# Optimization experiments

Hardware: AMD Instinct MI355X
Metric: run time of the kernel (lower is better)

Reference implementation:

```python
import jax, jax.numpy as jnp
import numpy as np

MAX_REL = 128  # max_relative_position


def setup_inputs() -> dict:
    key = jax.random.key(0)
    k1, k2, k3, k4 = jax.random.split(key, 4)
    B, H, S, D = 2, 8, 2048, 64
    q = jax.random.normal(k1, (B, H, S, D), dtype=jnp.float32)
    k = jax.random.normal(k2, (B, H, S, D), dtype=jnp.float32)
    v = jax.random.normal(k3, (B, H, S, D), dtype=jnp.float32)
    rel_table = jax.random.normal(k4, (2 * MAX_REL + 1, D), dtype=jnp.float32)
    return {"q": q, "k": k, "v": v, "rel_table": rel_table}


def reference(q, k, v, rel_table):
    B, H, S, D = q.shape
    scale = jnp.sqrt(jnp.asarray(D, q.dtype))
    # content scores: [B,H,S,S]
    qk_scores = jnp.einsum('bhqd,bhkd->bhqk', q, k)
    # relative position index matrix [S,S] clamped to [-MAX_REL, MAX_REL]
    pos = jnp.arange(S)
    rel_idx = jnp.clip(pos[None, :] - pos[:, None], -MAX_REL, MAX_REL) + MAX_REL
    rel_emb = rel_table[rel_idx]  # [S,S,D]
    # relative scores: per-query dot with rel embedding row -> [B,H,S,S]
    rel_scores = jnp.einsum('bhqd,qkd->bhqk', q, rel_emb)
    scores = (qk_scores + rel_scores) / scale
    attn = jax.nn.softmax(scores, axis=-1)
    # output: [B,H,S,D]
    return jnp.einsum('bhqk,bhkd->bhqd', attn, v)
```

## Files before the change

kernel.cpp:

```cpp
#include <hip/hip_runtime.h>

typedef _Float16 half8 __attribute__((ext_vector_type(8)));
typedef _Float16 half4 __attribute__((ext_vector_type(4)));
typedef float f32x4 __attribute__((ext_vector_type(4)));

#define S_LEN 2048
#define HDIM 64
#define QBLK 64
#define KVBLK 64
#define NT (S_LEN / KVBLK)
#define QRS 258
#define NBH 16
#define L2E 1.44269504f
#define TSTR 72

__device__ __forceinline__ void load_lds16(const void* g, void* l) {
    __builtin_amdgcn_global_load_lds(
        (const __attribute__((address_space(1))) unsigned int*)g,
        (__attribute__((address_space(3))) unsigned int*)l, 16, 0, 0);
}

__global__ __launch_bounds__(256)
void convert_kv_kernel(const float* __restrict__ Kg, const float* __restrict__ Vg,
                       _Float16* __restrict__ Kh, _Float16* __restrict__ Vp)
{
    __shared__ _Float16 tile[KVBLK * TSTR];
    const int bid = blockIdx.x;
    const int tid = threadIdx.x;
    if (bid < 1024) {
        const int id = bid * 256 + tid;
        const int r  = id >> 3;
        const int d0 = (id & 7) * 8;
        const float* src = Kg + (size_t)r * HDIM + d0;
        f32x4 f0 = *(const f32x4*)(src);
        f32x4 f1 = *(const f32x4*)(src + 4);
        half8 h;
#pragma unroll
        for (int j = 0; j < 4; ++j) { h[j] = (_Float16)f0[j]; h[j+4] = (_Float16)f1[j]; }
        const int bh = r >> 11, kvg = r & 2047;
        const int t = kvg >> 6, kv = kvg & 63;
        const size_t blk = (size_t)(bh * NT + t) * 8192;
        const int off = (kv * 128 + d0 * 2) ^ ((kv & 7) << 4);
        *(half8*)((char*)Kh + blk + off) = h;
    } else {
        const int bt = bid - 1024;
        const int bh = bt >> 5, t = bt & 31;
        {
            const int kv = tid >> 2;
            const int d0 = (tid & 3) * 16;
            const float* src = Vg + ((size_t)bh * S_LEN + t * KVBLK + kv) * HDIM + d0;
            f32x4 f0 = *(const f32x4*)(src);
            f32x4 f1 = *(const f32x4*)(src + 4);
            f32x4 f2 = *(const f32x4*)(src + 8);
            f32x4 f3 = *(const f32x4*)(src + 12);
            half8 h0, h1;
#pragma unroll
            for (int j = 0; j < 4; ++j) {
                h0[j] = (_Float16)f0[j]; h0[j+4] = (_Float16)f1[j];
                h1[j] = (_Float16)f2[j]; h1[j+4] = (_Float16)f3[j];
            }
            *(half8*)&tile[kv * TSTR + d0]     = h0;
            *(half8*)&tile[kv * TSTR + d0 + 8] = h1;
        }
        __syncthreads();
        {
            const int dp = tid >> 2;
            const int u0 = (tid & 3) * 2;
            char* base = (char*)Vp + (size_t)bt * 8192;
            const int dsw = (dp & 7) << 4;
#pragma unroll
            for (int ui = 0; ui < 2; ++ui) {
                const int u  = u0 + ui;
                const int kc = u >> 2, gg = u & 3;
                half8 ch;
#pragma unroll
                for (int r = 0; r < 4; ++r) {
                    ch[r]     = tile[(32*kc + 4*gg + r)      * TSTR + dp];
                    ch[4 + r] = tile[(32*kc + 16 + 4*gg + r) * TSTR + dp];
                }
                *(half8*)(base + ((dp * 128 + u * 16) ^ dsw)) = ch;
            }
        }
    }
}

__global__ __launch_bounds__(512, 4)
void relattn_v8(const float* __restrict__ Qg, const float* __restrict__ RELg,
                const _Float16* __restrict__ Kh, const _Float16* __restrict__ Vp,
                float* __restrict__ Og)
{
    __shared__ __attribute__((aligned(16))) _Float16 Kbuf[3][4096];
    __shared__ __attribute__((aligned(16))) _Float16 Vbuf[2][4096];
    __shared__ __attribute__((aligned(16))) _Float16 Qrel[QBLK * QRS];
    __shared__ float MLds[2][64];
    __shared__ float LLds[2][64];

    const int tid  = threadIdx.x;
    const int wave = tid >> 6;
    const int lane = tid & 63;
    const int c  = lane & 15;
    const int g  = lane >> 4;
    const int qs = wave & 3;
    const int ks = wave >> 2;

    const int wk = ((blockIdx.x & 7) << 6) + (blockIdx.x >> 3);
    const int bh = wk >> 5;
    const int q0 = (wk & 31) * QBLK;
    const size_t hoff = (size_t)bh * S_LEN * HDIM;

    const char* kimg = (const char*)Kh + (size_t)bh * NT * 8192;
    const char* vimg = (const char*)Vp + (size_t)bh * NT * 8192;

    load_lds16(vimg + tid * 16, (char*)Vbuf + tid * 16);
    load_lds16(kimg + tid * 16, (char*)Kbuf + tid * 16);
    load_lds16(kimg + 8192 + tid * 16, (char*)&Kbuf[1][0] + tid * 16);

    const int qb0 = q0 + 16 * qs;
    half8 bq[2];
#pragma unroll
    for (int kc = 0; kc < 2; ++kc) {
        const float* src = Qg + hoff + (size_t)(qb0 + c) * HDIM + kc * 32 + g * 8;
        f32x4 f0 = *(const f32x4*)(src);
        f32x4 f1 = *(const f32x4*)(src + 4);
        half8 h;
#pragma unroll
        for (int j = 0; j < 4; ++j) {
            h[j]     = (_Float16)(f0[j] * 0.125f);
            h[j + 4] = (_Float16)(f1[j] * 0.125f);
        }
        bq[kc] = h;
    }

    if (ks == 0) {
#pragma unroll 1
        for (int t = 0; t < 17; ++t) {
            f32x4 acc = {0.f, 0.f, 0.f, 0.f};
            int r = t * 16 + c;
            if (r > 256) r = 256;
#pragma unroll
            for (int kc = 0; kc < 2; ++kc) {
                const float* src = RELg + (size_t)r * HDIM + kc * 32 + g * 8;
                f32x4 f0 = *(const f32x4*)(src);
                f32x4 f1 = *(const f32x4*)(src + 4);
                half8 b;
#pragma unroll
                for (int j = 0; j < 4; ++j) { b[j] = (_Float16)f0[j]; b[j+4] = (_Float16)f1[j]; }
                acc = __builtin_amdgcn_mfma_f32_16x16x32_f16(bq[kc], b, acc, 0, 0, 0);
            }
            const int col = t * 16 + c;
            if (col <= 256) {
#pragma unroll
                for (int reg = 0; reg < 4; ++reg)
                    Qrel[(16 * qs + 4 * g + reg) * QRS + col] = (_Float16)acc[reg];
            }
        }
    }
    __syncthreads();

    const _Float16* qr = &Qrel[(16 * qs + c) * QRS];
    const float bias_lo = (float)qr[0];
    const float bias_hi = (float)qr[256];

    const int swz = (c & 7) << 4;
    int akoff[2][2], voff[4];
#pragma unroll
    for (int n = 0; n < 2; ++n)
#pragma unroll
        for (int kc = 0; kc < 2; ++kc)
            akoff[n][kc] = (((32 * ks + 16 * n + c) * 128) + kc * 64 + g * 16) ^ swz;
#pragma unroll
    for (int dn = 0; dn < 4; ++dn)
        voff[dn] = (((16 * dn + c) * 128) + ks * 64 + g * 16) ^ swz;

    half8 ones;
#pragma unroll
    for (int j = 0; j < 8; ++j) ones[j] = (_Float16)1.0f;

    float m = -1e30f;
    f32x4 l_acc = {0.f, 0.f, 0.f, 0.f};
    f32x4 oacc[4];
#pragma unroll
    for (int i = 0; i < 4; ++i) oacc[i] = (f32x4){0.f, 0.f, 0.f, 0.f};

#define BODY(t, KB, VB, VBN, KBN) do {                                               \
        asm volatile("s_waitcnt vmcnt(1)" ::: "memory");                             \
        __builtin_amdgcn_s_barrier();                                                \
        {                                                                            \
            const int tv = ((t) + 1 < NT) ? (t) + 1 : NT - 1;                        \
            const int tk = ((t) + 2 < NT) ? (t) + 2 : NT - 1;                        \
            load_lds16(vimg + (size_t)tv * 8192 + tid * 16,                          \
                       (char*)&Vbuf[VBN][0] + tid * 16);                             \
            load_lds16(kimg + (size_t)tk * 8192 + tid * 16,                          \
                       (char*)&Kbuf[KBN][0] + tid * 16);                             \
        }                                                                            \
        const char* kb = (const char*)&Kbuf[KB][0];                                  \
        const char* vb = (const char*)&Vbuf[VB][0];                                  \
        const int kws = (t) * KVBLK + 32 * ks;                                       \
        half8 a00 = *(const half8*)(kb + akoff[0][0]);                               \
        half8 a01 = *(const half8*)(kb + akoff[0][1]);                               \
        half8 a10 = *(const half8*)(kb + akoff[1][0]);                               \
        half8 a11 = *(const half8*)(kb + akoff[1][1]);                               \
        f32x4 s0 = {0.f,0.f,0.f,0.f}, s1 = {0.f,0.f,0.f,0.f};                        \
        __builtin_amdgcn_s_setprio(1);                                               \
        s0 = __builtin_amdgcn_mfma_f32_16x16x32_f16(a00, bq[0], s0, 0, 0, 0);        \
        s1 = __builtin_amdgcn_mfma_f32_16x16x32_f16(a10, bq[0], s1, 0, 0, 0);        \
        s0 = __builtin_amdgcn_mfma_f32_16x16x32_f16(a01, bq[1], s0, 0, 0, 0);        \
        s1 = __builtin_amdgcn_mfma_f32_16x16x32_f16(a11, bq[1], s1, 0, 0, 0);        \
        __builtin_amdgcn_s_setprio(0);                                               \
        float bias = 0.f;                                                            \
        float lm;                                                                    \
        if (kws + 159 <= qb0) {                                                      \
            bias = bias_lo;                                                          \
            lm = fmaxf(fmaxf(fmaxf(s0[0], s0[1]), fmaxf(s0[2], s0[3])),              \
                       fmaxf(fmaxf(s1[0], s1[1]), fmaxf(s1[2], s1[3]))) + bias;      \
        } else if (kws >= qb0 + 143) {                                               \
            bias = bias_hi;                                                          \
            lm = fmaxf(fmaxf(fmaxf(s0[0], s0[1]), fmaxf(s0[2], s0[3])),              \
                       fmaxf(fmaxf(s1[0], s1[1]), fmaxf(s1[2], s1[3]))) + bias;      \
        } else {                                                                     \
            const int base_d = kws + 4 * g - (qb0 + c) + 128;                        \
            _Pragma("unroll")                                                        \
            for (int r = 0; r < 4; ++r) {                                            \
                int i0 = base_d + r;                                                 \
                i0 = i0 < 0 ? 0 : (i0 > 256 ? 256 : i0);                             \
                int i1 = base_d + 16 + r;                                            \
                i1 = i1 < 0 ? 0 : (i1 > 256 ? 256 : i1);                             \
                s0[r] += (float)qr[i0];                                              \
                s1[r] += (float)qr[i1];                                              \
            }                                                                        \
            lm = fmaxf(fmaxf(fmaxf(s0[0], s0[1]), fmaxf(s0[2], s0[3])),              \
                       fmaxf(fmaxf(s1[0], s1[1]), fmaxf(s1[2], s1[3])));             \
        }                                                                            \
        if (!__all(lm <= m + 8.f)) {                                                 \
            float mt = lm;                                                           \
            mt = fmaxf(mt, __shfl_xor(mt, 16, 64));                                  \
            mt = fmaxf(mt, __shfl_xor(mt, 32, 64));                                  \
            const float mnew = fmaxf(m, mt);                                         \
            const float al = __builtin_amdgcn_exp2f((m - mnew) * L2E);               \
            m = mnew;                                                                \
            _Pragma("unroll")                                                        \
            for (int r = 0; r < 4; ++r) {                                            \
                const float ar = __shfl(al, 20 * g + r, 64);                         \
                l_acc[r] *= ar;                                                      \
                _Pragma("unroll")                                                    \
                for (int dn = 0; dn < 4; ++dn) oacc[dn][r] *= ar;                    \
            }                                                                        \
        }                                                                            \
        const float fold = (bias - m) * L2E;                                         \
        half8 ap;                                                                    \
        _Pragma("unroll")                                                            \
        for (int r = 0; r < 4; ++r) {                                                \
            ap[r]     = (_Float16)__builtin_amdgcn_exp2f(fmaf(s0[r], L2E, fold));    \
            ap[4 + r] = (_Float16)__builtin_amdgcn_exp2f(fmaf(s1[r], L2E, fold));    \
        }                                                                            \
        half8 v0 = *(const half8*)(vb + voff[0]);                                    \
        half8 v1 = *(const half8*)(vb + voff[1]);                                    \
        half8 v2 = *(const half8*)(vb + voff[2]);                                    \
        half8 v3 = *(const half8*)(vb + voff[3]);                                    \
        __builtin_amdgcn_s_setprio(1);                                               \
        l_acc   = __builtin_amdgcn_mfma_f32_16x16x32_f16(ap, ones, l_acc, 0, 0, 0);  \
        oacc[0] = __builtin_amdgcn_mfma_f32_16x16x32_f16(ap, v0, oacc[0], 0, 0, 0);  \
        oacc[1] = __builtin_amdgcn_mfma_f32_16x16x32_f16(ap, v1, oacc[1], 0, 0, 0);  \
        oacc[2] = __builtin_amdgcn_mfma_f32_16x16x32_f16(ap, v2, oacc[2], 0, 0, 0);  \
        oacc[3] = __builtin_amdgcn_mfma_f32_16x16x32_f16(ap, v3, oacc[3], 0, 0, 0);  \
        __builtin_amdgcn_s_setprio(0);                                               \
    } while (0)

#pragma unroll 1
    for (int tt = 0; tt < 30; tt += 6) {
        BODY(tt + 0, 0, 0, 1, 2);
        BODY(tt + 1, 1, 1, 0, 0);
        BODY(tt + 2, 2, 0, 1, 1);
        BODY(tt + 3, 0, 1, 0, 2);
        BODY(tt + 4, 1, 0, 1, 0);
        BODY(tt + 5, 2, 1, 0, 1);
    }
    BODY(30, 0, 0, 1, 2);
    BODY(31, 1, 1, 0, 0);
#undef BODY

    asm volatile("s_waitcnt vmcnt(0)" ::: "memory");
    __syncthreads();

    {
        char* Ob = (char*)Kbuf;
#pragma unroll
        for (int r = 0; r < 4; ++r) {
            const int row = 16 * qs + 4 * g + r;
            const int rsw = (row & 7) << 4;
#pragma unroll
            for (int dn = 0; dn < 4; ++dn)
                *(_Float16*)(Ob + ks * 8192 + ((row * 128 + (16 * dn + c) * 2) ^ rsw))
                    = (_Float16)oacc[dn][r];
        }
        if (g == 0) MLds[ks][16 * qs + c] = m;
        if (c == 0) {
#pragma unroll
            for (int r = 0; r < 4; ++r)
                LLds[ks][16 * qs + 4 * g + r] = l_acc[r];
        }
        __syncthreads();

        const int row = 16 * qs + c;
        const int rsw = (c & 7) << 4;
        const float m0 = MLds[0][row], m1 = MLds[1][row];
        const float l0 = LLds[0][row], l1 = LLds[1][row];
        const float M  = fmaxf(m0, m1);
        const float w0 = __builtin_amdgcn_exp2f((m0 - M) * L2E);
        const float w1 = __builtin_amdgcn_exp2f((m1 - M) * L2E);
        const float inv = 1.0f / (l0 * w0 + l1 * w1);

        const int dof = 64 * ks + 16 * g;
        half8 o0 = *(const half8*)(Ob +        ((row * 128 + dof) ^ rsw));
        half8 o1 = *(const half8*)(Ob + 8192 + ((row * 128 + dof) ^ rsw));
        float* dst = Og + hoff + (size_t)(q0 + row) * HDIM + 32 * ks + 8 * g;
        f32x4 oA, oB;
#pragma unroll
        for (int j = 0; j < 4; ++j) {
            oA[j] = ((float)o0[j]     * w0 + (float)o1[j]     * w1) * inv;
            oB[j] = ((float)o0[4 + j] * w0 + (float)o1[4 + j] * w1) * inv;
        }
        *(f32x4*)dst = oA;
        *(f32x4*)(dst + 4) = oB;
    }
}

__global__ __launch_bounds__(256, 2)
void relattn_v1(const float* __restrict__ Qg, const float* __restrict__ Kg,
                const float* __restrict__ Vg, const float* __restrict__ RELg,
                float* __restrict__ Og)
{
    __shared__ _Float16 Klds[KVBLK * HDIM];
    __shared__ _Float16 Vt[HDIM * KVBLK];
    __shared__ _Float16 Plds[4][16 * KVBLK];
    __shared__ _Float16 Qrel[QBLK * QRS];

    const int tid  = threadIdx.x;
    const int wave = tid >> 6;
    const int lane = tid & 63;
    const int c = lane & 15;
    const int g = lane >> 4;

    const int bid = blockIdx.x;
    const int bh  = bid >> 5;
    const int q0  = (bid & 31) * QBLK;

    const size_t hoff = (size_t)bh * S_LEN * HDIM;
    const float* Qh = Qg + hoff;
    const float* Kh = Kg + hoff;
    const float* Vh = Vg + hoff;

    const int qrow_frag = q0 + wave * 16 + c;
    half8 aq[2];
#pragma unroll
    for (int kc = 0; kc < 2; ++kc) {
        const float* src = Qh + (size_t)qrow_frag * HDIM + kc * 32 + g * 8;
        f32x4 f0 = *(const f32x4*)(src);
        f32x4 f1 = *(const f32x4*)(src + 4);
        half8 h;
#pragma unroll
        for (int j = 0; j < 4; ++j) {
            h[j]     = (_Float16)(f0[j] * 0.125f);
            h[j + 4] = (_Float16)(f1[j] * 0.125f);
        }
        aq[kc] = h;
    }

#pragma unroll 1
    for (int t = 0; t < 17; ++t) {
        f32x4 acc = {0.f, 0.f, 0.f, 0.f};
        int r = t * 16 + c;
        if (r > 256) r = 256;
#pragma unroll
        for (int kc = 0; kc < 2; ++kc) {
            const float* src = RELg + (size_t)r * HDIM + kc * 32 + g * 8;
            f32x4 f0 = *(const f32x4*)(src);
            f32x4 f1 = *(const f32x4*)(src + 4);
            half8 b;
#pragma unroll
            for (int j = 0; j < 4; ++j) { b[j] = (_Float16)f0[j]; b[j+4] = (_Float16)f1[j]; }
            acc = __builtin_amdgcn_mfma_f32_16x16x32_f16(aq[kc], b, acc, 0, 0, 0);
        }
        const int col = t * 16 + c;
        if (col <= 256) {
#pragma unroll
            for (int reg = 0; reg < 4; ++reg)
                Qrel[(wave * 16 + 4 * g + reg) * QRS + col] = (_Float16)acc[reg];
        }
    }

    float mrow[4], lrow[4];
    f32x4 oacc[4];
#pragma unroll
    for (int i = 0; i < 4; ++i) {
        mrow[i] = -1e30f; lrow[i] = 0.f;
        oacc[i] = (f32x4){0.f, 0.f, 0.f, 0.f};
    }

    for (int k0 = 0; k0 < S_LEN; k0 += KVBLK) {
        __syncthreads();
        {
            const int r  = tid >> 2;
            const int dq = (tid & 3) << 4;
            const float* src = Kh + (size_t)(k0 + r) * HDIM + dq;
            f32x4 f0 = *(const f32x4*)(src);
            f32x4 f1 = *(const f32x4*)(src + 4);
            f32x4 f2 = *(const f32x4*)(src + 8);
            f32x4 f3 = *(const f32x4*)(src + 12);
            half8 h0, h1;
#pragma unroll
            for (int j = 0; j < 4; ++j) {
                h0[j] = (_Float16)f0[j]; h0[j+4] = (_Float16)f1[j];
                h1[j] = (_Float16)f2[j]; h1[j+4] = (_Float16)f3[j];
            }
            const int swz = (r & 7) << 4;
            char* base = (char*)Klds;
            *(half8*)(base + ((r * 128 + dq * 2) ^ swz))      = h0;
            *(half8*)(base + ((r * 128 + dq * 2 + 16) ^ swz)) = h1;
        }
        {
            const int kv = tid & 63;
            const int dbase = (tid >> 6) << 4;
            const float* src = Vh + (size_t)(k0 + kv) * HDIM + dbase;
            f32x4 f0 = *(const f32x4*)(src);
            f32x4 f1 = *(const f32x4*)(src + 4);
            f32x4 f2 = *(const f32x4*)(src + 8);
            f32x4 f3 = *(const f32x4*)(src + 12);
            float vals[16];
#pragma unroll
            for (int j = 0; j < 4; ++j) {
                vals[j] = f0[j]; vals[4+j] = f1[j]; vals[8+j] = f2[j]; vals[12+j] = f3[j];
            }
            char* base = (char*)Vt;
#pragma unroll
            for (int i = 0; i < 16; ++i) {
                const int d = dbase + i;
                const int off = (d * 128 + kv * 2) ^ ((d & 7) << 4);
                *(_Float16*)(base + off) = (_Float16)vals[i];
            }
        }
        __syncthreads();

        f32x4 sacc[4];
#pragma unroll
        for (int n = 0; n < 4; ++n) sacc[n] = (f32x4){0.f,0.f,0.f,0.f};
#pragma unroll
        for (int kc = 0; kc < 2; ++kc) {
#pragma unroll
            for (int n = 0; n < 4; ++n) {
                const int off = (((16*n + c) * 128) + kc * 64 + g * 16) ^ ((c & 7) << 4);
                half8 bk = *(const half8*)((const char*)Klds + off);
                sacc[n] = __builtin_amdgcn_mfma_f32_16x16x32_f16(aq[kc], bk, sacc[n], 0, 0, 0);
            }
        }

        float sval[4][4];
        const int myq0 = q0 + wave * 16 + 4 * g;
#pragma unroll
        for (int n = 0; n < 4; ++n) {
            const int kpos = k0 + 16 * n + c;
#pragma unroll
            for (int reg = 0; reg < 4; ++reg) {
                int rel = kpos - (myq0 + reg);
                rel = rel < -128 ? -128 : (rel > 128 ? 128 : rel);
                const float bias = (float)Qrel[(wave*16 + 4*g + reg) * QRS + (rel + 128)];
                sval[n][reg] = sacc[n][reg] + bias;
            }
        }

        float mt[4];
#pragma unroll
        for (int reg = 0; reg < 4; ++reg) {
            float mp = fmaxf(fmaxf(sval[0][reg], sval[1][reg]),
                             fmaxf(sval[2][reg], sval[3][reg]));
#pragma unroll
            for (int msk = 1; msk < 16; msk <<= 1)
                mp = fmaxf(mp, __shfl_xor(mp, msk, 64));
            mt[reg] = mp;
        }

        float alpha[4], psum[4];
#pragma unroll
        for (int reg = 0; reg < 4; ++reg) {
            const float mn = fmaxf(mrow[reg], mt[reg]);
            alpha[reg] = __expf(mrow[reg] - mn);
            mrow[reg] = mn;
            psum[reg] = 0.f;
        }

        char* pbase = (char*)&Plds[wave][0];
#pragma unroll
        for (int n = 0; n < 4; ++n) {
#pragma unroll
            for (int reg = 0; reg < 4; ++reg) {
                const float pv = __expf(sval[n][reg] - mrow[reg]);
                psum[reg] += pv;
                const int row = 4 * g + reg;
                const int off = (row * 128 + (16 * n + c) * 2) ^ ((row & 7) << 4);
                *(_Float16*)(pbase + off) = (_Float16)pv;
            }
        }

#pragma unroll
        for (int reg = 0; reg < 4; ++reg) {
            float ps = psum[reg];
#pragma unroll
            for (int msk = 1; msk < 16; msk <<= 1)
                ps += __shfl_xor(ps, msk, 64);
            lrow[reg] = lrow[reg] * alpha[reg] + ps;
#pragma unroll
            for (int dn = 0; dn < 4; ++dn) oacc[dn][reg] *= alpha[reg];
        }

        asm volatile("s_waitcnt lgkmcnt(0)" ::: "memory");

        half8 ap[2];
#pragma unroll
        for (int kc = 0; kc < 2; ++kc) {
            const int off = (c * 128 + kc * 64 + g * 16) ^ ((c & 7) << 4);
            ap[kc] = *(const half8*)(pbase + off);
        }
#pragma unroll
        for (int kc = 0; kc < 2; ++kc) {
#pragma unroll
            for (int dn = 0; dn < 4; ++dn) {
                const int drow = 16 * dn + c;
                const int off = (drow * 128 + kc * 64 + g * 16) ^ ((c & 7) << 4);
                half8 bv = *(const half8*)((const char*)Vt + off);
                oacc[dn] = __builtin_amdgcn_mfma_f32_16x16x32_f16(ap[kc], bv, oacc[dn], 0, 0, 0);
            }
        }
    }

#pragma unroll
    for (int reg = 0; reg < 4; ++reg) {
        const float inv = 1.0f / lrow[reg];
        const int row = q0 + wave * 16 + 4 * g + reg;
        float* dst = Og + hoff + (size_t)row * HDIM + c;
#pragma unroll
        for (int dn = 0; dn < 4; ++dn)
            dst[16 * dn] = oacc[dn][reg] * inv;
    }
}

extern "C" void kernel_launch(void* const* d_in, const int* in_sizes, int n_in,
                              void* d_out, int out_size, void* d_ws, size_t ws_size,
                              hipStream_t stream) {
    const float* q   = (const float*)d_in[0];
    const float* k   = (const float*)d_in[1];
    const float* v   = (const float*)d_in[2];
    const float* rel = (const float*)d_in[3];
    float* out = (float*)d_out;
    (void)in_sizes; (void)n_in; (void)out_size;

    const size_t kv_bytes = (size_t)NBH * S_LEN * HDIM * sizeof(_Float16);
    if (ws_size >= 2 * kv_bytes) {
        _Float16* KhB = (_Float16*)d_ws;
        _Float16* VpB = (_Float16*)((char*)d_ws + kv_bytes);
        convert_kv_kernel<<<dim3(1536), 256, 0, stream>>>(k, v, KhB, VpB);
        relattn_v8<<<dim3(NBH * (S_LEN / QBLK)), 512, 0, stream>>>(q, rel, KhB, VpB, out);
    } else {
        relattn_v1<<<dim3(NBH * (S_LEN / QBLK)), 256, 0, stream>>>(q, k, v, rel, out);
    }
}
```

Measured before the change: 58.96 us.

## Precompute Q·rel in separate kernel and split attention into smaller query blocks

```diff
diff --git a/kernel.cpp b/kernel.cpp
--- a/kernel.cpp
+++ b/kernel.cpp
@@ -6,9 +6,7 @@
 
 #define S_LEN 2048
 #define HDIM 64
-#define QBLK 64
-#define KVBLK 64
-#define NT (S_LEN / KVBLK)
+#define NT (S_LEN / 64)
 #define QRS 258
 #define NBH 16
 #define L2E 1.44269504f
@@ -24,7 +22,7 @@
 void convert_kv_kernel(const float* __restrict__ Kg, const float* __restrict__ Vg,
                        _Float16* __restrict__ Kh, _Float16* __restrict__ Vp)
 {
-    __shared__ _Float16 tile[KVBLK * TSTR];
+    __shared__ _Float16 tile[64 * TSTR];
     const int bid = blockIdx.x;
     const int tid = threadIdx.x;
     if (bid < 1024) {
@@ -48,7 +46,7 @@
         {
             const int kv = tid >> 2;
             const int d0 = (tid & 3) * 16;
-            const float* src = Vg + ((size_t)bh * S_LEN + t * KVBLK + kv) * HDIM + d0;
+            const float* src = Vg + ((size_t)bh * S_LEN + t * 64 + kv) * HDIM + d0;
             f32x4 f0 = *(const f32x4*)(src);
             f32x4 f1 = *(const f32x4*)(src + 4);
             f32x4 f2 = *(const f32x4*)(src + 8);
@@ -81,6 +79,250 @@
                 *(half8*)(base + ((dp * 128 + u * 16) ^ dsw)) = ch;
             }
         }
+    }
+}
+
+__global__ __launch_bounds__(256)
+void qrel_kernel(const float* __restrict__ Qg, const float* __restrict__ RELg,
+                 _Float16* __restrict__ Qrel_g)
+{
+    const int b = blockIdx.x;
+    const int tid = threadIdx.x;
+    const int wave = tid >> 6;
+    const int lane = tid & 63;
+    const int c = lane & 15, g = lane >> 4;
+
+    const int row = b * 64 + wave * 16 + c;
+    half8 aq[2];
+#pragma unroll
+    for (int kc = 0; kc < 2; ++kc) {
+        const float* src = Qg + (size_t)row * HDIM + kc * 32 + g * 8;
+        f32x4 f0 = *(const f32x4*)(src);
+        f32x4 f1 = *(const f32x4*)(src + 4);
+        half8 h;
+#pragma unroll
+        for (int j = 0; j < 4; ++j) {
+            h[j]     = (_Float16)(f0[j] * 0.125f);
+            h[j + 4] = (_Float16)(f1[j] * 0.125f);
+        }
+        aq[kc] = h;
+    }
+#pragma unroll 1
+    for (int t = 0; t < 17; ++t) {
+        f32x4 acc = {0.f, 0.f, 0.f, 0.f};
+        int r = t * 16 + c;
+        if (r > 256) r = 256;
+#pragma unroll
+        for (int kc = 0; kc < 2; ++kc) {
+            const float* src = RELg + (size_t)r * HDIM + kc * 32 + g * 8;
+            f32x4 f0 = *(const f32x4*)(src);
+            f32x4 f1 = *(const f32x4*)(src + 4);
+            half8 bb;
+#pragma unroll
+            for (int j = 0; j < 4; ++j) { bb[j] = (_Float16)f0[j]; bb[j+4] = (_Float16)f1[j]; }
+            acc = __builtin_amdgcn_mfma_f32_16x16x32_f16(aq[kc], bb, acc, 0, 0, 0);
+        }
+        const int col = t * 16 + c;
+        if (col <= 256) {
+#pragma unroll
+            for (int reg = 0; reg < 4; ++reg)
+                Qrel_g[(size_t)(b * 64 + wave * 16 + 4 * g + reg) * QRS + col] = (_Float16)acc[reg];
+        }
+    }
+}
+
+__global__ __launch_bounds__(512, 8)
+void relattn_v12(const float* __restrict__ Qg, const _Float16* __restrict__ Qrel_g,
+                 const _Float16* __restrict__ Kh, const _Float16* __restrict__ Vp,
+                 float* __restrict__ Og)
+{
+    __shared__ __attribute__((aligned(16))) _Float16 Kbuf[2][4096];
+    __shared__ __attribute__((aligned(16))) _Float16 Vbuf[2][4096];
+    __shared__ float MLm[8][16];
+    __shared__ float MLl[8][16];
+
+    const int tid  = threadIdx.x;
+    const int wave = tid >> 6;
+    const int lane = tid & 63;
+    const int c  = lane & 15;
+    const int g  = lane >> 4;
+    const int qs = wave >> 2;
+    const int ks = wave & 3;
+
+    const int wk  = ((blockIdx.x & 7) << 7) + (blockIdx.x >> 3);
+    const int bh  = wk >> 6;
+    const int q0b = (wk & 63) * 32;
+    const size_t hoff = (size_t)bh * S_LEN * HDIM;
+
+    const char* kimg = (const char*)Kh + (size_t)bh * NT * 8192;
+    const char* vimg = (const char*)Vp + (size_t)bh * NT * 8192;
+
+    load_lds16(kimg + tid * 16, (char*)&Kbuf[0][0] + tid * 16);
+    load_lds16(vimg + tid * 16, (char*)&Vbuf[0][0] + tid * 16);
+
+    const int qrow = q0b + 16 * qs + c;
+    half8 bq[2];
+#pragma unroll
+    for (int kc = 0; kc < 2; ++kc) {
+        const float* src = Qg + hoff + (size_t)qrow * HDIM + kc * 32 + g * 8;
+        f32x4 f0 = *(const f32x4*)(src);
+        f32x4 f1 = *(const f32x4*)(src + 4);
+        half8 h;
+#pragma unroll
+        for (int j = 0; j < 4; ++j) {
+            h[j]     = (_Float16)(f0[j] * 0.125f);
+            h[j + 4] = (_Float16)(f1[j] * 0.125f);
+        }
+        bq[kc] = h;
+    }
+
+    const _Float16* qrp = Qrel_g + (size_t)(bh * S_LEN + qrow) * QRS;
+    const float bias_lo = (float)qrp[0];
+    const float bias_hi = (float)qrp[256];
+
+    const int r64 = 16 * ks + c;
+    int koff[2];
+#pragma unroll
+    for (int kc = 0; kc < 2; ++kc)
+        koff[kc] = (r64 * 128 + kc * 64 + g * 16) ^ ((r64 & 7) << 4);
+    int voff[4];
+#pragma unroll
+    for (int dn = 0; dn < 4; ++dn) {
+        const int d = 16 * dn + c;
+        voff[dn] = (d * 128 + (4 * (ks >> 1) + g) * 16 + 8 * (ks & 1)) ^ ((d & 7) << 4);
+    }
+
+    float m = -1e30f, l = 0.f;
+    f32x4 oacc[4];
+#pragma unroll
+    for (int i = 0; i < 4; ++i) oacc[i] = (f32x4){0.f, 0.f, 0.f, 0.f};
+
+#pragma unroll 1
+    for (int t = 0; t < NT; ++t) {
+        const int b = t & 1;
+        asm volatile("s_waitcnt vmcnt(0)" ::: "memory");
+        __builtin_amdgcn_s_barrier();
+        {
+            const int tn = (t + 1 < NT) ? t + 1 : t;
+            load_lds16(kimg + (size_t)tn * 8192 + tid * 16, (char*)&Kbuf[b ^ 1][0] + tid * 16);
+            load_lds16(vimg + (size_t)tn * 8192 + tid * 16, (char*)&Vbuf[b ^ 1][0] + tid * 16);
+        }
+
+        const char* kb = (const char*)&Kbuf[b][0];
+        half8 a0 = *(const half8*)(kb + koff[0]);
+        half8 a1 = *(const half8*)(kb + koff[1]);
+        f32x4 sacc = {0.f, 0.f, 0.f, 0.f};
+        __builtin_amdgcn_s_setprio(1);
+        sacc = __builtin_amdgcn_mfma_f32_16x16x32_f16(a0, bq[0], sacc, 0, 0, 0);
+        sacc = __builtin_amdgcn_mfma_f32_16x16x32_f16(a1, bq[1], sacc, 0, 0, 0);
+        __builtin_amdgcn_s_setprio(0);
+
+        float bias, lm;
+        if (64 * t + 192 <= q0b) {
+            bias = bias_lo;
+            lm = fmaxf(fmaxf(sacc[0], sacc[1]), fmaxf(sacc[2], sacc[3])) + bias;
+        } else if (64 * t >= q0b + 159) {
+            bias = bias_hi;
+            lm = fmaxf(fmaxf(sacc[0], sacc[1]), fmaxf(sacc[2], sacc[3])) + bias;
+        } else {
+            bias = 0.f;
+            const int base_d = 64 * t + 16 * ks + 4 * g - qrow + 128;
+            lm = -1e30f;
+#pragma unroll
+            for (int r = 0; r < 4; ++r) {
+                int idx = base_d + r;
+                idx = idx < 0 ? 0 : (idx > 256 ? 256 : idx);
+                sacc[r] += (float)qrp[idx];
+                lm = fmaxf(lm, sacc[r]);
+            }
+        }
+        lm = fmaxf(lm, __shfl_xor(lm, 16, 64));
+        lm = fmaxf(lm, __shfl_xor(lm, 32, 64));
+        if (!__all(lm <= m + 8.f)) {
+            const float mnew = fmaxf(m, lm);
+            const float al = __builtin_amdgcn_exp2f((m - mnew) * L2E);
+            m = mnew;
+            l *= al;
+#pragma unroll
+            for (int r = 0; r < 4; ++r) {
+                const float ar = __shfl(al, 4 * g + r, 64);
+#pragma unroll
+                for (int dn = 0; dn < 4; ++dn) oacc[dn][r] *= ar;
+            }
+        }
+        const float fold = (bias - m) * L2E;
+        half4 ap;
+        float ps = 0.f;
+#pragma unroll
+        for (int r = 0; r < 4; ++r) {
+            const float pv = __builtin_amdgcn_exp2f(fmaf(sacc[r], L2E, fold));
+            ps += pv;
+            ap[r] = (_Float16)pv;
+        }
+        ps += __shfl_xor(ps, 16, 64);
+        ps += __shfl_xor(ps, 32, 64);
+        l += ps;
+
+        const char* vb = (const char*)&Vbuf[b][0];
+        half4 v0 = *(const half4*)(vb + voff[0]);
+        half4 v1 = *(const half4*)(vb + voff[1]);
+        half4 v2 = *(const half4*)(vb + voff[2]);
+        half4 v3 = *(const half4*)(vb + voff[3]);
+        __builtin_amdgcn_s_setprio(1);
+        oacc[0] = __builtin_amdgcn_mfma_f32_16x16x16f16(ap, v0, oacc[0], 0, 0, 0);
+        oacc[1] = __builtin_amdgcn_mfma_f32_16x16x16f16(ap, v1, oacc[1], 0, 0, 0);
+        oacc[2] = __builtin_amdgcn_mfma_f32_16x16x16f16(ap, v2, oacc[2], 0, 0, 0);
+        oacc[3] = __builtin_amdgcn_mfma_f32_16x16x16f16(ap, v3, oacc[3], 0, 0, 0);
+        __builtin_amdgcn_s_setprio(0);
+    }
+
+    asm volatile("s_waitcnt vmcnt(0)" ::: "memory");
+    __syncthreads();
+    {
+        char* Ob = (char*)&Kbuf[0][0];
+#pragma unroll
+        for (int r = 0; r < 4; ++r) {
+            const int q = 16 * qs + 4 * g + r;
+            const int qsw = (q & 7) << 4;
+#pragma unroll
+            for (int dn = 0; dn < 4; ++dn) {
+                const int d = 16 * dn + c;
+                *(_Float16*)(Ob + ks * 4096 + q * 128 + ((d * 2) ^ qsw)) = (_Float16)oacc[dn][r];
+            }
+        }
+        if (g == 0) { MLm[wave][c] = m; MLl[wave][c] = l; }
+        __syncthreads();
+
+        const int q  = tid >> 4;
+        const int d0 = (tid & 15) * 4;
+        const int qs_ = q >> 4, qc = q & 15;
+        const int qsw = (q & 7) << 4;
+        float mm[4], ll[4];
+#pragma unroll
+        for (int k4 = 0; k4 < 4; ++k4) {
+            mm[k4] = MLm[4 * qs_ + k4][qc];
+            ll[k4] = MLl[4 * qs_ + k4][qc];
+        }
+        const float M = fmaxf(fmaxf(mm[0], mm[1]), fmaxf(mm[2], mm[3]));
+        float wgt[4], den = 0.f;
+#pragma unroll
+        for (int k4 = 0; k4 < 4; ++k4) {
+            wgt[k4] = __builtin_amdgcn_exp2f((mm[k4] - M) * L2E);
+            den += wgt[k4] * ll[k4];
+        }
+        const float inv = 1.0f / den;
+        float acc[4] = {0.f, 0.f, 0.f, 0.f};
+        const char* Obr = (const char*)&Kbuf[0][0] + q * 128;
+#pragma unroll
+        for (int k4 = 0; k4 < 4; ++k4) {
+            half4 o = *(const half4*)(Obr + k4 * 4096 + ((d0 * 2) ^ qsw));
+#pragma unroll
+            for (int j = 0; j < 4; ++j) acc[j] += (float)o[j] * wgt[k4];
+        }
+        f32x4 out;
+#pragma unroll
+        for (int j = 0; j < 4; ++j) out[j] = acc[j] * inv;
+        *(f32x4*)(Og + hoff + (size_t)(q0b + q) * HDIM + d0) = out;
     }
 }
 
@@ -91,7 +333,7 @@
 {
     __shared__ __attribute__((aligned(16))) _Float16 Kbuf[3][4096];
     __shared__ __attribute__((aligned(16))) _Float16 Vbuf[2][4096];
-    __shared__ __attribute__((aligned(16))) _Float16 Qrel[QBLK * QRS];
+    __shared__ __attribute__((aligned(16))) _Float16 Qrel[64 * QRS];
     __shared__ float MLds[2][64];
     __shared__ float LLds[2][64];
 
@@ -105,7 +347,7 @@
 
     const int wk = ((blockIdx.x & 7) << 6) + (blockIdx.x >> 3);
     const int bh = wk >> 5;
-    const int q0 = (wk & 31) * QBLK;
+    const int q0 = (wk & 31) * 64;
     const size_t hoff = (size_t)bh * S_LEN * HDIM;
 
     const char* kimg = (const char*)Kh + (size_t)bh * NT * 8192;
@@ -195,7 +437,7 @@
         }                                                                            \
         const char* kb = (const char*)&Kbuf[KB][0];                                  \
         const char* vb = (const char*)&Vbuf[VB][0];                                  \
-        const int kws = (t) * KVBLK + 32 * ks;                                       \
+        const int kws = (t) * 64 + 32 * ks;                                          \
         half8 a00 = *(const half8*)(kb + akoff[0][0]);                               \
         half8 a01 = *(const half8*)(kb + akoff[0][1]);                               \
         half8 a10 = *(const half8*)(kb + akoff[1][0]);                               \
@@ -281,7 +523,6 @@
 
     asm volatile("s_waitcnt vmcnt(0)" ::: "memory");
     __syncthreads();
-
     {
         char* Ob = (char*)Kbuf;
 #pragma unroll
@@ -330,10 +571,10 @@
                 const float* __restrict__ Vg, const float* __restrict__ RELg,
                 float* __restrict__ Og)
 {
-    __shared__ _Float16 Klds[KVBLK * HDIM];
-    __shared__ _Float16 Vt[HDIM * KVBLK];
-    __shared__ _Float16 Plds[4][16 * KVBLK];
-    __shared__ _Float16 Qrel[QBLK * QRS];
+    __shared__ _Float16 Klds[64 * HDIM];
+    __shared__ _Float16 Vt[HDIM * 64];
+    __shared__ _Float16 Plds[4][16 * 64];
+    __shared__ _Float16 Qrel[64 * QRS];
 
     const int tid  = threadIdx.x;
     const int wave = tid >> 6;
@@ -343,7 +584,7 @@
 
     const int bid = blockIdx.x;
     const int bh  = bid >> 5;
-    const int q0  = (bid & 31) * QBLK;
+    const int q0  = (bid & 31) * 64;
 
     const size_t hoff = (size_t)bh * S_LEN * HDIM;
     const float* Qh = Qg + hoff;
@@ -397,7 +638,7 @@
         oacc[i] = (f32x4){0.f, 0.f, 0.f, 0.f};
     }
 
-    for (int k0 = 0; k0 < S_LEN; k0 += KVBLK) {
+    for (int k0 = 0; k0 < S_LEN; k0 += 64) {
         __syncthreads();
         {
             const int r  = tid >> 2;
@@ -553,13 +794,24 @@
     float* out = (float*)d_out;
     (void)in_sizes; (void)n_in; (void)out_size;
 
-    const size_t kv_bytes = (size_t)NBH * S_LEN * HDIM * sizeof(_Float16);
-    if (ws_size >= 2 * kv_bytes) {
+    const size_t kv_bytes   = (size_t)NBH * S_LEN * HDIM * sizeof(_Float16);
+    const size_t qrel_bytes = (size_t)NBH * S_LEN * QRS * sizeof(_Float16);
+    const size_t need_full  = 2 * kv_bytes + qrel_bytes;
+
+    if (ws_size >= need_full) {
+        char* p = (char*)d_ws;
+        _Float16* KhB = (_Float16*)p;   p += kv_bytes;
+        _Float16* VpB = (_Float16*)p;   p += kv_bytes;
+        _Float16* QrB = (_Float16*)p;
+        convert_kv_kernel<<<dim3(1536), 256, 0, stream>>>(k, v, KhB, VpB);
+        qrel_kernel<<<dim3(512), 256, 0, stream>>>(q, rel, QrB);
+        relattn_v12<<<dim3(1024), 512, 0, stream>>>(q, QrB, KhB, VpB, out);
+    } else if (ws_size >= 2 * kv_bytes) {
         _Float16* KhB = (_Float16*)d_ws;
         _Float16* VpB = (_Float16*)((char*)d_ws + kv_bytes);
         convert_kv_kernel<<<dim3(1536), 256, 0, stream>>>(k, v, KhB, VpB);
-        relattn_v8<<<dim3(NBH * (S_LEN / QBLK)), 512, 0, stream>>>(q, rel, KhB, VpB, out);
+        relattn_v8<<<dim3(512), 512, 0, stream>>>(q, rel, KhB, VpB, out);
     } else {
-        relattn_v1<<<dim3(NBH * (S_LEN / QBLK)), 256, 0, stream>>>(q, k, v, rel, out);
+        relattn_v1<<<dim3(512), 256, 0, stream>>>(q, k, v, rel, out);
     }
 }
```

Result: slower. 87.62 us (+48.6%).
